# Kernel optimization log

Measured on AMD Instinct MI355X. Metric: run time of the kernel, lower is better.

## Reference

```python
import jax, jax.numpy as jnp
import numpy as np

LEAKY_SLOPE = 0.2
LN_EPS = 1e-5
SOFTMAX_EPS = 1e-16  # PyG softmax denominator eps


def setup_inputs() -> dict:
    key = jax.random.key(0)
    ks = jax.random.split(key, 8)
    N, E, F, H, C, ED = 100000, 1600000, 64, 8, 8, 16
    s = 1.0 / np.sqrt(F)
    return {
        "x": jax.random.normal(ks[0], (N, F), jnp.float32),
        "edge_index": jax.random.randint(ks[1], (2, E), 0, N, jnp.int32),
        "edge_attr": jax.random.normal(ks[2], (E, ED), jnp.float32),
        "W_l": jax.random.normal(ks[3], (H * C, F), jnp.float32) * s,
        "b_l": jnp.zeros((H * C,), jnp.float32),
        "W_r": jax.random.normal(ks[4], (H * C, F), jnp.float32) * s,
        "b_r": jnp.zeros((H * C,), jnp.float32),
        "W_e": jax.random.normal(ks[5], (H * C, ED), jnp.float32) * (1.0 / np.sqrt(ED)),
        "att": jax.random.normal(ks[6], (1, H, C), jnp.float32) * (1.0 / np.sqrt(C)),
        "bias": jnp.zeros((H * C,), jnp.float32),
        "gamma": jnp.ones((F,), jnp.float32),
        "beta": jnp.zeros((F,), jnp.float32),
    }


def reference(x, edge_index, edge_attr, W_l, b_l, W_r, b_r, W_e, att, bias, gamma, beta):
    N, F = x.shape
    H, C = att.shape[1], att.shape[2]
    src, dst = edge_index[0], edge_index[1]  # PyG: row0=source(j), row1=target(i)

    xl = (x @ W_l.T + b_l).reshape(N, H, C)   # lin_l -> x_j side
    xr = (x @ W_r.T + b_r).reshape(N, H, C)   # lin_r -> x_i side
    e = (edge_attr @ W_e.T).reshape(-1, H, C)  # lin_edge (no bias)

    m = jax.nn.leaky_relu(xl[src] + xr[dst] + e, LEAKY_SLOPE)  # [E,H,C]
    logits = jnp.einsum('ehc,hc->eh', m, att[0])               # [E,H]

    # per-destination segment softmax
    mx = jax.ops.segment_max(logits, dst, num_segments=N)      # [N,H]
    mx = jnp.where(jnp.isfinite(mx), mx, 0.0)                  # nodes w/o in-edges
    ex = jnp.exp(logits - mx[dst])
    denom = jax.ops.segment_sum(ex, dst, num_segments=N)
    alpha = ex / (denom[dst] + SOFTMAX_EPS)                    # [E,H]; dropout is identity in eval

    agg = jax.ops.segment_sum(alpha[:, :, None] * xl[src], dst, num_segments=N)  # [N,H,C]
    out = agg.reshape(N, H * C) + bias

    h = out + x  # residual
    mu = jnp.mean(h, axis=-1, keepdims=True)
    var = jnp.mean((h - mu) ** 2, axis=-1, keepdims=True)
    hn = (h - mu) * jax.lax.rsqrt(var + LN_EPS) * gamma + beta
    return jax.nn.relu(hn)
```

## Files before the change

### kernel.cpp

```cpp
#include <hip/hip_runtime.h>

#define LEAKY 0.2f
#define LN_EPS 1e-5f
#define SM_EPS 1e-16f
#define CAP 64
#define WPAD 68

#define BIN_SHIFT 8
#define MAXBINS   448
#define CHUNK_A   7168
#define BCAP      5120

__global__ __launch_bounds__(256) void k_node_linear(
    const float* __restrict__ x,
    const float* __restrict__ Wl,
    const float* __restrict__ bl,
    const float* __restrict__ Wr,
    const float* __restrict__ br,
    float* __restrict__ xl, float* __restrict__ xr, int N)
{
    __shared__ __align__(16) float sW[64 * WPAD];

    const int tid = threadIdx.x;
    const int side = blockIdx.x & 1;
    const float* __restrict__ W  = side ? Wr : Wl;
    const float* __restrict__ bv = side ? br : bl;
    float* __restrict__ dst      = side ? xr : xl;

    for (int i = tid; i < 4096; i += 256)
        sW[(i >> 6) * WPAD + (i & 63)] = W[i];
    __syncthreads();

    const int lane = tid & 63;
    float4 wq[16];
    #pragma unroll
    for (int q = 0; q < 16; ++q)
        wq[q] = *(const float4*)&sW[lane * WPAD + q * 4];
    const float bb = bv[lane];

    const int stream0 = (blockIdx.x >> 1) * 4 + (tid >> 6);
    const int nstream = (gridDim.x >> 1) * 4;
    for (int n = stream0; n < N; n += nstream) {
        const float4* xrow = (const float4*)(x + (long long)n * 64);
        float a = bb;
        #pragma unroll
        for (int q = 0; q < 16; ++q) {
            const float4 xv = xrow[q];
            const float4 w  = wq[q];
            a = fmaf(xv.x, w.x, fmaf(xv.y, w.y, fmaf(xv.z, w.z, fmaf(xv.w, w.w, a))));
        }
        dst[(long long)n * 64 + lane] = a;
    }
}

__global__ __launch_bounds__(256) void k_bucket(
    const int* __restrict__ ei, int* __restrict__ deg,
    int* __restrict__ slot, int E)
{
    const int e = blockIdx.x * 256 + threadIdx.x;
    if (e >= E) return;
    const int dst = ei[E + e];
    const int pos = atomicAdd(deg + dst, 1);
    if (pos < CAP) slot[(long long)dst * CAP + pos] = e;
}

__global__ __launch_bounds__(256) void k_binA(
    const int* __restrict__ ei,
    int* __restrict__ binCnt,
    int2* __restrict__ binArr,
    int E, int nbins)
{
    __shared__ int2 ord[CHUNK_A];
    __shared__ int cnt[MAXBINS], offs[MAXBINS], cur[MAXBINS], resB[MAXBINS];

    const int tid  = threadIdx.x;
    const int lane = tid & 63;
    const int ebase = blockIdx.x * CHUNK_A;
    const int nE = (E - ebase < CHUNK_A) ? (E - ebase) : CHUNK_A;
    const int* __restrict__ dstp = ei + E + ebase;

    for (int b = tid; b < MAXBINS; b += 256) { cnt[b] = 0; cur[b] = 0; }
    __syncthreads();

    for (int i = tid; i < nE; i += 256)
        atomicAdd(&cnt[dstp[i] >> BIN_SHIFT], 1);
    __syncthreads();

    if (tid < 64) {
        int carry = 0;
        #pragma unroll
        for (int seg = 0; seg < MAXBINS / 64; ++seg) {
            const int v = cnt[seg * 64 + lane];
            int s = v;
            #pragma unroll
            for (int off = 1; off < 64; off <<= 1) {
                const int t = __shfl_up(s, off, 64);
                if (lane >= off) s += t;
            }
            offs[seg * 64 + lane] = carry + s - v;
            carry += __shfl(s, 63, 64);
        }
    }
    __syncthreads();

    for (int i = tid; i < nE; i += 256) {
        const int d = dstp[i];
        const int b = d >> BIN_SHIFT;
        const int pos = atomicAdd(&cur[b], 1);
        ord[offs[b] + pos] = make_int2(ebase + i, d);
    }
    __syncthreads();

    for (int b = tid; b < nbins; b += 256) {
        const int c = cnt[b];
        resB[b] = c ? atomicAdd(&binCnt[b], c) : 0;
    }
    __syncthreads();

    for (int i = tid; i < nE; i += 256) {
        const int2 p = ord[i];
        const int b = p.y >> BIN_SHIFT;
        const int k = resB[b] + (i - offs[b]);
        if (k < BCAP) binArr[(long long)b * BCAP + k] = p;
    }
}

__global__ __launch_bounds__(256) void k_binB(
    const int* __restrict__ binCnt,
    const int2* __restrict__ binArr,
    int* __restrict__ deg,
    int* __restrict__ slot,
    int N)
{
    __shared__ int ord2[BCAP];
    __shared__ int cnt2[256], offs2[256], cur2[256];

    const int b = blockIdx.x;
    const int tid  = threadIdx.x;
    const int lane = tid & 63;
    const int dst0 = b << BIN_SHIFT;
    int nb = binCnt[b];
    if (nb > BCAP) nb = BCAP;
    const int2* __restrict__ src = binArr + (long long)b * BCAP;

    cnt2[tid] = 0; cur2[tid] = 0;
    __syncthreads();

    for (int i = tid; i < nb; i += 256)
        atomicAdd(&cnt2[src[i].y - dst0], 1);
    __syncthreads();

    if (tid < 64) {
        int carry = 0;
        #pragma unroll
        for (int seg = 0; seg < 4; ++seg) {
            const int v = cnt2[seg * 64 + lane];
            int s = v;
            #pragma unroll
            for (int off = 1; off < 64; off <<= 1) {
                const int t = __shfl_up(s, off, 64);
                if (lane >= off) s += t;
            }
            offs2[seg * 64 + lane] = carry + s - v;
            carry += __shfl(s, 63, 64);
        }
    }
    __syncthreads();

    for (int i = tid; i < nb; i += 256) {
        const int2 p = src[i];
        const int d = p.y - dst0;
        const int pos = atomicAdd(&cur2[d], 1);
        ord2[offs2[d] + pos] = p.x;
    }
    __syncthreads();

    const int nd = (N - dst0 < 256) ? (N - dst0) : 256;
    if (tid < nd) deg[dst0 + tid] = cnt2[tid];

    const int wv = tid >> 6;
    for (int d = wv; d < nd; d += 4) {
        int c = cnt2[d];
        if (c > CAP) c = CAP;
        if (lane < c) slot[(long long)(dst0 + d) * CAP + lane] = ord2[offs2[d] + lane];
    }
}

__global__ __launch_bounds__(256) void k_gather(
    const int* __restrict__ ei,
    const float* __restrict__ ea,
    const float* __restrict__ We,
    const float* __restrict__ att,
    const float* __restrict__ xl, const float* __restrict__ xr,
    const int* __restrict__ deg, const int* __restrict__ slot,
    const float* __restrict__ x,
    const float* __restrict__ bias, const float* __restrict__ gamma,
    const float* __restrict__ beta,
    float* __restrict__ out, int N)
{
    const int lane = threadIdx.x & 63;
    const int n = blockIdx.x * 4 + (threadIdx.x >> 6);
    if (n >= N) return;

    const float4* w4 = (const float4*)(We + lane * 16);
    const float4 w0 = w4[0], w1 = w4[1], w2 = w4[2], w3 = w4[3];
    const float attv = att[lane];
    const float xrv = xr[(long long)n * 64 + lane];

    const int d = min(deg[n], CAP);

    int veid = 0, vsrc = 0;
    if (lane < d) {
        veid = slot[(long long)n * CAP + lane];
        vsrc = ei[veid];
    }

    float acc = 0.f;
    float ns  = 0.f;

    float xlA = 0.f, xlB = 0.f;
    float4 a0, a1, a2, a3, b0, b1, b2, b3;
    a0 = a1 = a2 = a3 = b0 = b1 = b2 = b3 = make_float4(0.f, 0.f, 0.f, 0.f);

#define FETCH(j, XLV, E0, E1, E2, E3) do {                       \
        const int s_ = __shfl(vsrc, (j), 64);                    \
        const int e_ = __shfl(veid, (j), 64);                    \
        XLV = xl[(long long)s_ * 64 + lane];                     \
        const float4* p_ = (const float4*)(ea + (long long)e_ * 16); \
        E0 = p_[0]; E1 = p_[1]; E2 = p_[2]; E3 = p_[3];          \
    } while (0)

    if (d > 0) FETCH(0, xlA, a0, a1, a2, a3);
    if (d > 1) FETCH(1, xlB, b0, b1, b2, b3);

    for (int i = 0; i < d; ++i) {
        const float xlc = xlA;
        const float4 c0 = a0, c1 = a1, c2 = a2, c3 = a3;
        xlA = xlB; a0 = b0; a1 = b1; a2 = b2; a3 = b3;
        if (i + 2 < d) FETCH(i + 2, xlB, b0, b1, b2, b3);

        float ep = c0.x*w0.x + c0.y*w0.y + c0.z*w0.z + c0.w*w0.w
                 + c1.x*w1.x + c1.y*w1.y + c1.z*w1.z + c1.w*w1.w
                 + c2.x*w2.x + c2.y*w2.y + c2.z*w2.z + c2.w*w2.w
                 + c3.x*w3.x + c3.y*w3.y + c3.z*w3.z + c3.w*w3.w;
        float m = xlc + xrv + ep;
        m = (m > 0.f) ? m : LEAKY * m;
        float p = m * attv;
        p += __shfl_xor(p, 1, 64);
        p += __shfl_xor(p, 2, 64);
        p += __shfl_xor(p, 4, 64);
        const float ex = __expf(p);
        ns  += ex;
        acc = fmaf(ex, xlc, acc);
    }
#undef FETCH

    const float a = acc / (ns + SM_EPS);
    const float hv = a + bias[lane] + x[(long long)n * 64 + lane];

    float s = hv;
    #pragma unroll
    for (int off = 32; off; off >>= 1) s += __shfl_xor(s, off, 64);
    const float mu = s * (1.f / 64.f);
    const float dd = hv - mu;
    float v = dd * dd;
    #pragma unroll
    for (int off = 32; off; off >>= 1) v += __shfl_xor(v, off, 64);
    const float var = v * (1.f / 64.f);

    float hn = dd * rsqrtf(var + LN_EPS) * gamma[lane] + beta[lane];
    out[(long long)n * 64 + lane] = (hn > 0.f) ? hn : 0.f;
}

extern "C" void kernel_launch(void* const* d_in, const int* in_sizes, int n_in,
                              void* d_out, int out_size, void* d_ws, size_t ws_size,
                              hipStream_t stream) {
    (void)n_in; (void)out_size;

    const float* x     = (const float*)d_in[0];
    const int*   ei    = (const int*)d_in[1];
    const float* ea    = (const float*)d_in[2];
    const float* Wl    = (const float*)d_in[3];
    const float* bl    = (const float*)d_in[4];
    const float* Wr    = (const float*)d_in[5];
    const float* br    = (const float*)d_in[6];
    const float* We    = (const float*)d_in[7];
    const float* att   = (const float*)d_in[8];
    const float* bias  = (const float*)d_in[9];
    const float* gamma = (const float*)d_in[10];
    const float* beta  = (const float*)d_in[11];

    const int N = in_sizes[0] / 64;
    const int E = in_sizes[1] / 2;
    const int nbins = (N + (1 << BIN_SHIFT) - 1) >> BIN_SHIFT;

    float* w = (float*)d_ws;
    float* xl   = w;                      w += (size_t)N * 64;
    float* xr   = w;                      w += (size_t)N * 64;
    int* deg    = (int*)w;
    int* binCnt = deg + N;
    int* slot   = binCnt + MAXBINS;
    int2* binArr = (int2*)(slot + (size_t)N * CAP);
    const size_t needed = ((char*)(binArr + (size_t)nbins * BCAP)) - (char*)d_ws;

    float* out = (float*)d_out;

    const bool binned = (nbins <= MAXBINS) && (ws_size >= needed);

    hipMemsetAsync(deg, 0, ((size_t)N + MAXBINS) * sizeof(int), stream);

    k_node_linear<<<2048, 256, 0, stream>>>(x, Wl, bl, Wr, br, xl, xr, N);

    if (binned) {
        const int nbA = (E + CHUNK_A - 1) / CHUNK_A;
        k_binA<<<nbA, 256, 0, stream>>>(ei, binCnt, binArr, E, nbins);
        k_binB<<<nbins, 256, 0, stream>>>(binCnt, binArr, deg, slot, N);
    } else {
        k_bucket<<<(E + 255) / 256, 256, 0, stream>>>(ei, deg, slot, E);
    }

    k_gather<<<(N + 3) / 4, 256, 0, stream>>>(
        ei, ea, We, att, xl, xr, deg, slot, x, bias, gamma, beta, out, N);
}
```

Measured before the change: 629.7 us.

## Carry source index through binning so gather skips dependent edge_index load

The binning pipeline now packs the edge id plus the low destination bits into one int and carries the source node alongside it, so the CSR slot array stores (edge, src) pairs. The gather kernel no longer does a dependent random load of edge_index[0][eid] before fetching xl. In exchange, slot storage doubles, k_binA derives each element's bin with a binary search over offsets, and BCAP shrinks to fit the larger shared buffer. The binned path is now limited to E up to 2^21.

```diff
diff --git a/kernel.cpp b/kernel.cpp
--- a/kernel.cpp
+++ b/kernel.cpp
@@ -9,7 +9,8 @@
 #define BIN_SHIFT 8
 #define MAXBINS   448
 #define CHUNK_A   7168
-#define BCAP      5120
+#define BCAP      4608
+#define EMASK     0x1FFFFF
 
 __global__ __launch_bounds__(256) void k_node_linear(
     const float* __restrict__ x,
@@ -55,13 +56,13 @@
 
 __global__ __launch_bounds__(256) void k_bucket(
     const int* __restrict__ ei, int* __restrict__ deg,
-    int* __restrict__ slot, int E)
+    int2* __restrict__ slot2, int E)
 {
     const int e = blockIdx.x * 256 + threadIdx.x;
     if (e >= E) return;
     const int dst = ei[E + e];
     const int pos = atomicAdd(deg + dst, 1);
-    if (pos < CAP) slot[(long long)dst * CAP + pos] = e;
+    if (pos < CAP) slot2[(long long)dst * CAP + pos] = make_int2(e, ei[e]);
 }
 
 __global__ __launch_bounds__(256) void k_binA(
@@ -78,6 +79,7 @@
     const int ebase = blockIdx.x * CHUNK_A;
     const int nE = (E - ebase < CHUNK_A) ? (E - ebase) : CHUNK_A;
     const int* __restrict__ dstp = ei + E + ebase;
+    const int* __restrict__ srcp = ei + ebase;
 
     for (int b = tid; b < MAXBINS; b += 256) { cnt[b] = 0; cur[b] = 0; }
     __syncthreads();
@@ -107,7 +109,8 @@
         const int d = dstp[i];
         const int b = d >> BIN_SHIFT;
         const int pos = atomicAdd(&cur[b], 1);
-        ord[offs[b] + pos] = make_int2(ebase + i, d);
+        ord[offs[b] + pos] =
+            make_int2((ebase + i) | ((d & ((1 << BIN_SHIFT) - 1)) << 21), srcp[i]);
     }
     __syncthreads();
 
@@ -119,9 +122,14 @@
 
     for (int i = tid; i < nE; i += 256) {
         const int2 p = ord[i];
-        const int b = p.y >> BIN_SHIFT;
-        const int k = resB[b] + (i - offs[b]);
-        if (k < BCAP) binArr[(long long)b * BCAP + k] = p;
+        const int b = ((unsigned)p.x >> 21) + 0;
+        int lo = 0, hi = nbins;
+        while (hi - lo > 1) {
+            const int mid = (lo + hi) >> 1;
+            if (offs[mid] <= i) lo = mid; else hi = mid;
+        }
+        const int k = resB[lo] + (i - offs[lo]);
+        if (k < BCAP) binArr[(long long)lo * BCAP + k] = p;
     }
 }
 
@@ -129,10 +137,10 @@
     const int* __restrict__ binCnt,
     const int2* __restrict__ binArr,
     int* __restrict__ deg,
-    int* __restrict__ slot,
+    int2* __restrict__ slot2,
     int N)
 {
-    __shared__ int ord2[BCAP];
+    __shared__ int2 ord2[BCAP];
     __shared__ int cnt2[256], offs2[256], cur2[256];
 
     const int b = blockIdx.x;
@@ -147,7 +155,7 @@
     __syncthreads();
 
     for (int i = tid; i < nb; i += 256)
-        atomicAdd(&cnt2[src[i].y - dst0], 1);
+        atomicAdd(&cnt2[((unsigned)src[i].x >> 21) & 0xFF], 1);
     __syncthreads();
 
     if (tid < 64) {
@@ -169,9 +177,9 @@
 
     for (int i = tid; i < nb; i += 256) {
         const int2 p = src[i];
-        const int d = p.y - dst0;
+        const int d = ((unsigned)p.x >> 21) & 0xFF;
         const int pos = atomicAdd(&cur2[d], 1);
-        ord2[offs2[d] + pos] = p.x;
+        ord2[offs2[d] + pos] = make_int2(p.x & EMASK, p.y);
     }
     __syncthreads();
 
@@ -182,17 +190,16 @@
     for (int d = wv; d < nd; d += 4) {
         int c = cnt2[d];
         if (c > CAP) c = CAP;
-        if (lane < c) slot[(long long)(dst0 + d) * CAP + lane] = ord2[offs2[d] + lane];
+        if (lane < c) slot2[(long long)(dst0 + d) * CAP + lane] = ord2[offs2[d] + lane];
     }
 }
 
 __global__ __launch_bounds__(256) void k_gather(
-    const int* __restrict__ ei,
     const float* __restrict__ ea,
     const float* __restrict__ We,
     const float* __restrict__ att,
     const float* __restrict__ xl, const float* __restrict__ xr,
-    const int* __restrict__ deg, const int* __restrict__ slot,
+    const int* __restrict__ deg, const int2* __restrict__ slot2,
     const float* __restrict__ x,
     const float* __restrict__ bias, const float* __restrict__ gamma,
     const float* __restrict__ beta,
@@ -211,8 +218,9 @@
 
     int veid = 0, vsrc = 0;
     if (lane < d) {
-        veid = slot[(long long)n * CAP + lane];
-        vsrc = ei[veid];
+        const int2 es = slot2[(long long)n * CAP + lane];
+        veid = es.x;
+        vsrc = es.y;
     }
 
     float acc = 0.f;
@@ -299,13 +307,14 @@
     float* xr   = w;                      w += (size_t)N * 64;
     int* deg    = (int*)w;
     int* binCnt = deg + N;
-    int* slot   = binCnt + MAXBINS;
-    int2* binArr = (int2*)(slot + (size_t)N * CAP);
+    int2* slot2 = (int2*)(binCnt + MAXBINS);
+    int2* binArr = slot2 + (size_t)N * CAP;
     const size_t needed = ((char*)(binArr + (size_t)nbins * BCAP)) - (char*)d_ws;
 
     float* out = (float*)d_out;
 
-    const bool binned = (nbins <= MAXBINS) && (ws_size >= needed);
+    const bool binned = (nbins <= MAXBINS) && (E <= (1 << 21)) &&
+                        (ws_size >= needed);
 
     hipMemsetAsync(deg, 0, ((size_t)N + MAXBINS) * sizeof(int), stream);
 
@@ -314,11 +323,11 @@
     if (binned) {
         const int nbA = (E + CHUNK_A - 1) / CHUNK_A;
         k_binA<<<nbA, 256, 0, stream>>>(ei, binCnt, binArr, E, nbins);
-        k_binB<<<nbins, 256, 0, stream>>>(binCnt, binArr, deg, slot, N);
+        k_binB<<<nbins, 256, 0, stream>>>(binCnt, binArr, deg, slot2, N);
     } else {
-        k_bucket<<<(E + 255) / 256, 256, 0, stream>>>(ei, deg, slot, E);
+        k_bucket<<<(E + 255) / 256, 256, 0, stream>>>(ei, deg, slot2, E);
     }
 
     k_gather<<<(N + 3) / 4, 256, 0, stream>>>(
-        ei, ea, We, att, xl, xr, deg, slot, x, bias, gamma, beta, out, N);
-}
+        ea, We, att, xl, xr, deg, slot2, x, bias, gamma, beta, out, N);
+}
```

After: 650.6 us. 1.03x slower.
